# Kernel optimization log

Hardware: AMD Instinct MI355X
Metric: run time of the kernel (lower is better)

Reference implementation:

```python
import jax, jax.numpy as jnp
import numpy as np

KERNEL_SIZE = 5
GROUP_SIZE = 1
SCALE = 2


def setup_inputs() -> dict:
    key = jax.random.key(0)
    k1, k2 = jax.random.split(key)
    features = jax.random.normal(k1, (8, 256, 64, 64), dtype=jnp.float32)
    masks = jax.random.uniform(k2, (8, KERNEL_SIZE * KERNEL_SIZE * GROUP_SIZE, 64 * SCALE, 64 * SCALE), dtype=jnp.float32)
    return {"features": features, "masks": masks}


def _carafe_naive(features, masks, k, g, s):
    n, c, h, w = features.shape
    cg = c // g
    pad = (k - 1) // 2
    fp = jnp.pad(features, ((0, 0), (0, 0), (pad, pad), (pad, pad)))
    # im2col patches, matching F.unfold ordering: channel outer, kernel
    # positions row-major inner -> [n, c, k*k, h, w]
    patches = jnp.stack(
        [fp[:, :, i:i + h, j:j + w] for i in range(k) for j in range(k)],
        axis=2,
    )
    feat = patches.reshape(n, g, cg, k * k, h, w)          # n g c i h w
    ker = masks.reshape(n, g, k * k, h, s, w, s)           # n g i h a w b
    # per-pixel dynamic conv over the k*k window, fused with upsample
    out = jnp.einsum('ngcihw,ngihawb->ngchawb', feat, ker)  # n g c h a w b
    return out.reshape(n, c, h * s, w * s)


def reference(features, masks):
    return _carafe_naive(features, masks, KERNEL_SIZE, GROUP_SIZE, SCALE)
```

## Files before the change

kernel.cpp:

```cpp
#include <hip/hip_runtime.h>

#define K 5
#define N_ 8
#define C_ 256
#define H_ 64
#define W_ 64
#define HW (H_ * W_)
#define HO 128
#define WO 128
#define HOWO (HO * WO)
#define HB 4
#define WB 32
#define CCHUNK 32
#define UC 8
#define NGROUP (CCHUNK / UC)
#define LDS_R (HB + K - 1)
#define LDS_C (WB + K - 1)
#define POS (LDS_R * LDS_C)

__global__ __launch_bounds__(256)
void carafe_up_kernel(const float* __restrict__ feat,
                      const float* __restrict__ mask,
                      float* __restrict__ out) {
    const int wt = blockIdx.x;
    const int ht = blockIdx.y;
    const int zc = blockIdx.z;
    const int n  = zc >> 3;
    const int c0 = (zc & 7) * CCHUNK;
    const int h0 = ht * HB;
    const int w0 = wt * WB;

    const int tid        = threadIdx.x;
    const int wlocal_out = tid & 63;
    const int h_local    = tid >> 6;
    const int w_local    = wlocal_out >> 1;
    const int Wg         = w0 * 2 + wlocal_out;
    const int Hg0        = (h0 + h_local) * 2;

    float m0[K * K], m1[K * K];
    const float* mbase = mask + (size_t)n * (K * K) * HOWO
                              + (size_t)Hg0 * WO + Wg;
    #pragma unroll
    for (int i = 0; i < K * K; ++i) {
        m0[i] = mbase[(size_t)i * HOWO];
        m1[i] = mbase[(size_t)i * HOWO + WO];
    }

    int off0, off1;
    bool v0, v1, has1;
    {
        int p  = tid;
        int r  = p / LDS_C, cc = p - r * LDS_C;
        int hs = h0 - 2 + r, ws = w0 - 2 + cc;
        v0   = (hs >= 0 && hs < H_ && ws >= 0 && ws < W_);
        off0 = hs * W_ + ws;
    }
    has1 = (tid + 256) < POS;
    {
        int p  = tid + 256;
        int r  = p / LDS_C, cc = p - r * LDS_C;
        int hs = h0 - 2 + r, ws = w0 - 2 + cc;
        v1   = has1 && (hs >= 0 && hs < H_ && ws >= 0 && ws < W_);
        off1 = hs * W_ + ws;
    }

    __shared__ float4 lds[2][2][POS];

    const float* fbase = feat + (size_t)n * C_ * HW;
    float*       obase = out  + (size_t)n * C_ * HOWO
                              + (size_t)Hg0 * WO + Wg;

    float s0[UC], s1[UC];
    auto stage_load = [&](int cbase) {
        const float* fp = fbase + (size_t)cbase * HW;
        #pragma unroll
        for (int u = 0; u < UC; ++u) s0[u] = v0 ? fp[u * HW + off0] : 0.f;
        #pragma unroll
        for (int u = 0; u < UC; ++u) s1[u] = v1 ? fp[u * HW + off1] : 0.f;
    };
    auto stage_write = [&](int buf) {
        lds[buf][0][tid] = make_float4(s0[0], s0[1], s0[2], s0[3]);
        lds[buf][1][tid] = make_float4(s0[4], s0[5], s0[6], s0[7]);
        if (has1) {
            lds[buf][0][tid + 256] = make_float4(s1[0], s1[1], s1[2], s1[3]);
            lds[buf][1][tid + 256] = make_float4(s1[4], s1[5], s1[6], s1[7]);
        }
    };

    stage_load(c0);
    stage_write(0);
    __syncthreads();

    const int rbase = h_local * LDS_C + w_local;

    for (int g = 0; g < NGROUP; ++g) {
        const int buf = g & 1;

        if (g + 1 < NGROUP) stage_load(c0 + (g + 1) * UC);

        #pragma unroll
        for (int s = 0; s < 2; ++s) {
            const float4* Ls = &lds[buf][s][rbase];
            float a0x = 0.f, a0y = 0.f, a0z = 0.f, a0w = 0.f;
            float a1x = 0.f, a1y = 0.f, a1z = 0.f, a1w = 0.f;
            #pragma unroll
            for (int ki = 0; ki < K; ++ki) {
                #pragma unroll
                for (int kj = 0; kj < K; ++kj) {
                    float4 f  = Ls[ki * LDS_C + kj];
                    float  w0m = m0[ki * K + kj];
                    float  w1m = m1[ki * K + kj];
                    a0x = fmaf(f.x, w0m, a0x);  a1x = fmaf(f.x, w1m, a1x);
                    a0y = fmaf(f.y, w0m, a0y);  a1y = fmaf(f.y, w1m, a1y);
                    a0z = fmaf(f.z, w0m, a0z);  a1z = fmaf(f.z, w1m, a1z);
                    a0w = fmaf(f.w, w0m, a0w);  a1w = fmaf(f.w, w1m, a1w);
                }
            }
            float* oc = obase + (size_t)(c0 + g * UC + s * 4) * HOWO;
            __builtin_nontemporal_store(a0x, oc);
            __builtin_nontemporal_store(a1x, oc + WO);
            oc += HOWO;
            __builtin_nontemporal_store(a0y, oc);
            __builtin_nontemporal_store(a1y, oc + WO);
            oc += HOWO;
            __builtin_nontemporal_store(a0z, oc);
            __builtin_nontemporal_store(a1z, oc + WO);
            oc += HOWO;
            __builtin_nontemporal_store(a0w, oc);
            __builtin_nontemporal_store(a1w, oc + WO);
        }

        if (g + 1 < NGROUP) {
            stage_write(buf ^ 1);
            __syncthreads();
        }
    }
}

extern "C" void kernel_launch(void* const* d_in, const int* in_sizes, int n_in,
                              void* d_out, int out_size, void* d_ws, size_t ws_size,
                              hipStream_t stream) {
    const float* feat = (const float*)d_in[0];
    const float* mask = (const float*)d_in[1];
    float* out = (float*)d_out;

    dim3 grid(WO / (2 * WB), (HO / 2) / HB, N_ * (C_ / CCHUNK));
    dim3 block(256);
    carafe_up_kernel<<<grid, block, 0, stream>>>(feat, mask, out);
}
```

Before: 50.83 us.

## Compute a 2x2 output quad per thread with float2 masks and stores

Each thread now produces all four upsampled outputs for one source pixel instead of two, so every LDS feature read feeds twice as many FMAs. The tile height doubles to keep 256 threads per block, and masks and outputs use float2 vector loads and nontemporal stores. The aim is to cut LDS read traffic per FMA and make global memory accesses wider. In exchange each thread holds twice as many mask registers (100 floats), which may lower occupancy, and the grid has half as many blocks.

```diff
diff --git a/kernel.cpp b/kernel.cpp
--- a/kernel.cpp
+++ b/kernel.cpp
@@ -9,7 +9,7 @@
 #define HO 128
 #define WO 128
 #define HOWO (HO * WO)
-#define HB 4
+#define HB 8
 #define WB 32
 #define CCHUNK 32
 #define UC 8
@@ -18,10 +18,12 @@
 #define LDS_C (WB + K - 1)
 #define POS (LDS_R * LDS_C)
 
+typedef __attribute__((ext_vector_type(2))) float f2;
+
 __global__ __launch_bounds__(256)
-void carafe_up_kernel(const float* __restrict__ feat,
-                      const float* __restrict__ mask,
-                      float* __restrict__ out) {
+void carafe_quad_kernel(const float* __restrict__ feat,
+                        const float* __restrict__ mask,
+                        float* __restrict__ out) {
     const int wt = blockIdx.x;
     const int ht = blockIdx.y;
     const int zc = blockIdx.z;
@@ -30,36 +32,37 @@
     const int h0 = ht * HB;
     const int w0 = wt * WB;
 
-    const int tid        = threadIdx.x;
-    const int wlocal_out = tid & 63;
-    const int h_local    = tid >> 6;
-    const int w_local    = wlocal_out >> 1;
-    const int Wg         = w0 * 2 + wlocal_out;
-    const int Hg0        = (h0 + h_local) * 2;
+    const int tid = threadIdx.x;
+    const int r   = tid >> 5;
+    const int c   = tid & 31;
+    const int hb  = h0 + r;
+    const int wb  = w0 + c;
 
-    float m0[K * K], m1[K * K];
-    const float* mbase = mask + (size_t)n * (K * K) * HOWO
-                              + (size_t)Hg0 * WO + Wg;
-    #pragma unroll
-    for (int i = 0; i < K * K; ++i) {
-        m0[i] = mbase[(size_t)i * HOWO];
-        m1[i] = mbase[(size_t)i * HOWO + WO];
+    f2 m0[K * K], m1[K * K];
+    {
+        const f2* mb = (const f2*)(mask + (size_t)n * (K * K) * HOWO
+                                        + (size_t)(2 * hb) * WO + 2 * wb);
+        #pragma unroll
+        for (int i = 0; i < K * K; ++i) {
+            m0[i] = mb[(size_t)i * (HOWO / 2)];
+            m1[i] = mb[(size_t)i * (HOWO / 2) + WO / 2];
+        }
     }
 
     int off0, off1;
     bool v0, v1, has1;
     {
         int p  = tid;
-        int r  = p / LDS_C, cc = p - r * LDS_C;
-        int hs = h0 - 2 + r, ws = w0 - 2 + cc;
+        int rr = p / LDS_C, cc = p - rr * LDS_C;
+        int hs = h0 - 2 + rr, ws = w0 - 2 + cc;
         v0   = (hs >= 0 && hs < H_ && ws >= 0 && ws < W_);
         off0 = hs * W_ + ws;
     }
     has1 = (tid + 256) < POS;
     {
         int p  = tid + 256;
-        int r  = p / LDS_C, cc = p - r * LDS_C;
-        int hs = h0 - 2 + r, ws = w0 - 2 + cc;
+        int rr = p / LDS_C, cc = p - rr * LDS_C;
+        int hs = h0 - 2 + rr, ws = w0 - 2 + cc;
         v1   = has1 && (hs >= 0 && hs < H_ && ws >= 0 && ws < W_);
         off1 = hs * W_ + ws;
     }
@@ -68,7 +71,7 @@
 
     const float* fbase = feat + (size_t)n * C_ * HW;
     float*       obase = out  + (size_t)n * C_ * HOWO
-                              + (size_t)Hg0 * WO + Wg;
+                              + (size_t)(2 * hb) * WO + 2 * wb;
 
     float s0[UC], s1[UC];
     auto stage_load = [&](int cbase) {
@@ -91,7 +94,7 @@
     stage_write(0);
     __syncthreads();
 
-    const int rbase = h_local * LDS_C + w_local;
+    const int rbase = r * LDS_C + c;
 
     for (int g = 0; g < NGROUP; ++g) {
         const int buf = g & 1;
@@ -101,33 +104,28 @@
         #pragma unroll
         for (int s = 0; s < 2; ++s) {
             const float4* Ls = &lds[buf][s][rbase];
-            float a0x = 0.f, a0y = 0.f, a0z = 0.f, a0w = 0.f;
-            float a1x = 0.f, a1y = 0.f, a1z = 0.f, a1w = 0.f;
+            f2 a0[4], a1[4];
+            #pragma unroll
+            for (int u = 0; u < 4; ++u) { a0[u] = (f2)0.f; a1[u] = (f2)0.f; }
             #pragma unroll
             for (int ki = 0; ki < K; ++ki) {
                 #pragma unroll
                 for (int kj = 0; kj < K; ++kj) {
                     float4 f  = Ls[ki * LDS_C + kj];
-                    float  w0m = m0[ki * K + kj];
-                    float  w1m = m1[ki * K + kj];
-                    a0x = fmaf(f.x, w0m, a0x);  a1x = fmaf(f.x, w1m, a1x);
-                    a0y = fmaf(f.y, w0m, a0y);  a1y = fmaf(f.y, w1m, a1y);
-                    a0z = fmaf(f.z, w0m, a0z);  a1z = fmaf(f.z, w1m, a1z);
-                    a0w = fmaf(f.w, w0m, a0w);  a1w = fmaf(f.w, w1m, a1w);
+                    f2 w0m = m0[ki * K + kj];
+                    f2 w1m = m1[ki * K + kj];
+                    a0[0] += f.x * w0m;  a1[0] += f.x * w1m;
+                    a0[1] += f.y * w0m;  a1[1] += f.y * w1m;
+                    a0[2] += f.z * w0m;  a1[2] += f.z * w1m;
+                    a0[3] += f.w * w0m;  a1[3] += f.w * w1m;
                 }
             }
-            float* oc = obase + (size_t)(c0 + g * UC + s * 4) * HOWO;
-            __builtin_nontemporal_store(a0x, oc);
-            __builtin_nontemporal_store(a1x, oc + WO);
-            oc += HOWO;
-            __builtin_nontemporal_store(a0y, oc);
-            __builtin_nontemporal_store(a1y, oc + WO);
-            oc += HOWO;
-            __builtin_nontemporal_store(a0z, oc);
-            __builtin_nontemporal_store(a1z, oc + WO);
-            oc += HOWO;
-            __builtin_nontemporal_store(a0w, oc);
-            __builtin_nontemporal_store(a1w, oc + WO);
+            #pragma unroll
+            for (int u = 0; u < 4; ++u) {
+                f2* op = (f2*)(obase + (size_t)(c0 + g * UC + s * 4 + u) * HOWO);
+                __builtin_nontemporal_store(a0[u], op);
+                __builtin_nontemporal_store(a1[u], op + WO / 2);
+            }
         }
 
         if (g + 1 < NGROUP) {
@@ -144,7 +142,7 @@
     const float* mask = (const float*)d_in[1];
     float* out = (float*)d_out;
 
-    dim3 grid(WO / (2 * WB), (HO / 2) / HB, N_ * (C_ / CCHUNK));
+    dim3 grid(W_ / WB, H_ / HB, N_ * (C_ / CCHUNK));
     dim3 block(256);
-    carafe_up_kernel<<<grid, block, 0, stream>>>(feat, mask, out);
+    carafe_quad_kernel<<<grid, block, 0, stream>>>(feat, mask, out);
 }
```

New measurement: 45.90 us. 9.7% less time.
